# Kernel tuning notes

Measured on AMD Instinct MI355X. Metric: run time of the kernel, lower is better.

Reference implementation:

```python
import jax, jax.numpy as jnp
import numpy as np

MSA_DIM = 256
PAIR_DIM = 128
HEAD_DIM = 32


def setup_inputs() -> dict:
    key = jax.random.key(0)
    ks = jax.random.split(key, 9)
    n_seq, seq_len = 128, 256
    s = lambda d: 1.0 / np.sqrt(d)
    return {
        "msa_input": jax.random.normal(ks[0], (n_seq, seq_len, MSA_DIM), jnp.float32),
        "norm_w": jnp.ones((MSA_DIM,), jnp.float32),
        "norm_b": jnp.zeros((MSA_DIM,), jnp.float32),
        "w1": jax.random.normal(ks[1], (MSA_DIM, HEAD_DIM), jnp.float32) * s(MSA_DIM),
        "b1": jax.random.normal(ks[2], (HEAD_DIM,), jnp.float32) * 0.01,
        "w2": jax.random.normal(ks[3], (MSA_DIM, HEAD_DIM), jnp.float32) * s(MSA_DIM),
        "b2": jax.random.normal(ks[4], (HEAD_DIM,), jnp.float32) * 0.01,
        "w3": jax.random.normal(ks[5], (HEAD_DIM * HEAD_DIM, PAIR_DIM), jnp.float32) * s(HEAD_DIM * HEAD_DIM),
        "b3": jax.random.normal(ks[6], (PAIR_DIM,), jnp.float32) * 0.01,
    }


def _layernorm(x, w, b, eps=1e-5):
    mu = jnp.mean(x, axis=-1, keepdims=True)
    var = jnp.mean(jnp.square(x - mu), axis=-1, keepdims=True)
    return (x - mu) * jax.lax.rsqrt(var + eps) * w + b


def reference(msa_input, norm_w, norm_b, w1, b1, w2, b2, w3, b3):
    n_seq, seq_len, _ = msa_input.shape
    normed = _layernorm(msa_input, norm_w, norm_b)
    # proj_a uses linear2, proj_b uses linear1 (as in the torch code)
    proj_a = normed @ w2 + b2  # [n, i, c]
    proj_b = normed @ w1 + b1  # [n, j, c]
    # mean over MSA depth n expressed as a GEMM-style contraction
    outer = jnp.einsum('nia,njb->ijab', proj_a, proj_b) / n_seq  # [i, j, c, c]
    outer = outer.reshape(seq_len, seq_len, -1)
    return outer @ w3 + b3  # [i, j, pair_dim]
```

## Files before the change

kernel.cpp:

```cpp
#include <hip/hip_runtime.h>
#include <hip/hip_bf16.h>
#include <stdint.h>

#define SEQ  256
#define PD   128

typedef short bf16x8 __attribute__((ext_vector_type(8)));
typedef float f32x4  __attribute__((ext_vector_type(4)));
typedef float f32x16 __attribute__((ext_vector_type(16)));
typedef short s16x4  __attribute__((ext_vector_type(4)));

__device__ __forceinline__ short f2bf(float x) {
    union { float f; uint32_t u; } v; v.f = x;
    uint32_t r = v.u + 0x7FFFu + ((v.u >> 16) & 1u);
    return (short)(r >> 16);
}

__device__ __forceinline__ void gld16(const void* g, void* l) {
    __builtin_amdgcn_global_load_lds(
        (const __attribute__((address_space(1))) void*)g,
        (__attribute__((address_space(3))) void*)l, 16, 0, 0);
}

__global__ __launch_bounds__(256) void k_prep(const float* __restrict__ w1,
                                              const float* __restrict__ w2,
                                              const float* __restrict__ w3,
                                              short* __restrict__ w12t,
                                              short* __restrict__ w3p) {
    int id = blockIdx.x * 256 + threadIdx.x;
    if (id < 2048) {
        int col = id >> 5, cp = id & 31;
        int c = cp ^ (col & 7);
        bf16x8 o;
        #pragma unroll
        for (int e = 0; e < 8; ++e) {
            int k = c * 8 + e;
            float v = (col < 32) ? w2[k * 32 + col] : w1[k * 32 + (col - 32)];
            o[e] = f2bf(v);
        }
        *(bf16x8*)(w12t + id * 8) = o;
    } else {
        int id2 = id - 2048;
        int pg = id2 >> 12, ks = (id2 >> 6) & 63, l2 = id2 & 63;
        bf16x8 o;
        #pragma unroll
        for (int e = 0; e < 8; ++e) {
            int k = ks * 16 + (l2 >> 5) * 8 + e;
            int p = pg * 32 + (l2 & 31);
            o[e] = f2bf(w3[k * 128 + p]);
        }
        *(bf16x8*)(w3p + id2 * 8) = o;
    }
}

__global__ __launch_bounds__(256) void k_fused(const float* __restrict__ msa,
                                               const float* __restrict__ nw,
                                               const float* __restrict__ nb_,
                                               const float* __restrict__ b1,
                                               const float* __restrict__ b2,
                                               const short* __restrict__ w12t,
                                               short* __restrict__ pa,
                                               short* __restrict__ pb) {
    __shared__ short smem[32768];
    int i = blockIdx.x, nbk = blockIdx.y;
    int t = threadIdx.x, l = t & 63, w = t >> 6;

    #pragma unroll
    for (int it = 0; it < 8; ++it) {
        int ci = it * 256 + t;
        gld16(w12t + (size_t)ci * 8, smem + (it * 256 + (t & ~63)) * 8);
    }
    float4 x[16];
    const float* basep = msa + ((size_t)(nbk * 64 + w * 16) * SEQ + i) * 256 + l * 4;
    #pragma unroll
    for (int j = 0; j < 16; ++j)
        x[j] = *(const float4*)(basep + (size_t)j * SEQ * 256);
    float4 wv = *(const float4*)(nw + l * 4);
    float4 bv = *(const float4*)(nb_ + l * 4);
    #pragma unroll
    for (int j = 0; j < 16; ++j) {
        float s = x[j].x + x[j].y + x[j].z + x[j].w;
        #pragma unroll
        for (int o = 32; o > 0; o >>= 1) s += __shfl_xor(s, o, 64);
        float mu = s * (1.0f / 256.0f);
        float dx = x[j].x - mu, dy = x[j].y - mu, dz = x[j].z - mu, dw = x[j].w - mu;
        float sq = dx * dx + dy * dy + dz * dz + dw * dw;
        #pragma unroll
        for (int o = 32; o > 0; o >>= 1) sq += __shfl_xor(sq, o, 64);
        float rs = rsqrtf(sq * (1.0f / 256.0f) + 1e-5f);
        s16x4 o4;
        o4[0] = f2bf(dx * rs * wv.x + bv.x);
        o4[1] = f2bf(dy * rs * wv.y + bv.y);
        o4[2] = f2bf(dz * rs * wv.z + bv.z);
        o4[3] = f2bf(dw * rs * wv.w + bv.w);
        int row = w * 16 + j;
        *(s16x4*)((char*)smem + 32768 + row * 512 + (((l >> 1) ^ (row & 7)) * 16) + (l & 1) * 8) = o4;
    }
    __syncthreads();
    int lr = l & 15, lk = l >> 4;
    f32x4 acc[4] = {};
    #pragma unroll
    for (int ks = 0; ks < 8; ++ks) {
        int c = ks * 4 + lk;
        int xr = w * 16 + lr;
        bf16x8 xf = *(bf16x8*)((char*)smem + 32768 + xr * 512 + ((c ^ (xr & 7)) * 16));
        #pragma unroll
        for (int af = 0; af < 4; ++af) {
            int rw = af * 16 + lr;
            bf16x8 wf = *(bf16x8*)((char*)smem + rw * 512 + ((c ^ (rw & 7)) * 16));
            acc[af] = __builtin_amdgcn_mfma_f32_16x16x32_bf16(wf, xf, acc[af], 0, 0, 0);
        }
    }
    int nglob = nbk * 64 + w * 16 + lr;
    #pragma unroll
    for (int af = 0; af < 4; ++af) {
        #pragma unroll
        for (int r = 0; r < 4; ++r) {
            int cc = af * 16 + lk * 4 + r;
            float bias = (cc < 32) ? b2[cc] : b1[cc - 32];
            short v = f2bf(acc[af][r] + bias);
            if (cc < 32) pa[(size_t)(i * 32 + cc) * 128 + nglob] = v;
            else         pb[(size_t)(i * 32 + (cc - 32)) * 128 + nglob] = v;
        }
    }
}

__global__ __launch_bounds__(1024) void k_outer(const short* __restrict__ pa,
                                                const short* __restrict__ pb,
                                                const short* __restrict__ w3p,
                                                const float* __restrict__ b3,
                                                float* __restrict__ out) {
    __shared__ short smem[65536];
    int t = threadIdx.x, l = t & 63, w = t >> 6;
    int lin = blockIdx.x;
    int swz = (lin & 7) * 128 + (lin >> 3);
    int bi = swz >> 5, bj = swz & 31;

    const short* srcA = pa + (size_t)bi * 256 * 128;
    const short* srcB = pb + (size_t)bj * 256 * 128;
    #pragma unroll
    for (int it = 0; it < 8; ++it) {
        int ci = it * 1024 + t;
        int half = ci >> 12, rem = ci & 4095;
        int buf = rem >> 11, s = rem & 2047;
        int row = s >> 3, cl = s & 7;
        int gch = (cl ^ (row & 7)) + 8 * half;
        const short* g = (buf ? srcB : srcA) + row * 128 + gch * 8;
        gld16(g, smem + (it * 1024 + (t & ~63)) * 8);
    }
    __syncthreads();

    int wm = w & 3, wn = w >> 2;
    int lr = l & 15, lk = l >> 4;
    f32x4 acc1[4][4] = {};
    #pragma unroll
    for (int ks = 0; ks < 4; ++ks) {
        int c = ks * 4 + lk, half = c >> 3, cl = c & 7;
        bf16x8 af[4];
        #pragma unroll
        for (int mf = 0; mf < 4; ++mf) {
            int row = wm * 64 + mf * 16 + lr;
            af[mf] = *(bf16x8*)((char*)smem + half * 65536 + row * 128 + ((cl ^ (row & 7)) * 16));
        }
        #pragma unroll
        for (int nf = 0; nf < 4; ++nf) {
            int row = wn * 64 + nf * 16 + lr;
            bf16x8 bf = *(bf16x8*)((char*)smem + half * 65536 + 32768 + row * 128 + ((cl ^ (row & 7)) * 16));
            #pragma unroll
            for (int mf = 0; mf < 4; ++mf)
                acc1[nf][mf] = __builtin_amdgcn_mfma_f32_16x16x32_bf16(bf, af[mf], acc1[nf][mf], 0, 0, 0);
        }
    }
    __syncthreads();

    const float inv_n = 1.0f / 128.0f;
    #pragma unroll
    for (int nf = 0; nf < 4; ++nf) {
        #pragma unroll
        for (int mf = 0; mf < 4; ++mf) {
            int pair = (wm * 2 + (mf >> 1)) * 8 + (wn * 2 + (nf >> 1));
            int b = (nf & 1) * 16 + lk * 4;
            int q = lr * 4 + 2 * (nf & 1) + (lk >> 1);
            int qp = q ^ (pair & 7) ^ (((lr >> 1) & 3) << 1);
            s16x4 o;
            #pragma unroll
            for (int r = 0; r < 4; ++r) o[r] = f2bf(acc1[nf][mf][r] * inv_n);
            *(s16x4*)((char*)smem + (mf & 1) * 65536 + pair * 1024 + qp * 16 + (b & 7) * 2) = o;
        }
    }
    __syncthreads();

    f32x16 acc2[2] = {};
    int pg = w >> 1, kh = w & 1;
    if (w < 8) {
        #pragma unroll
        for (int ksi = 0; ksi < 32; ++ksi) {
            int ksg = kh * 32 + ksi;
            bf16x8 b2f = *(const bf16x8*)(w3p + ((size_t)(pg * 64 + ksg) * 64 + l) * 8);
            int q = (ksg & 31) * 2 + (l >> 5);
            int sa = (((ksg & 31) >> 2) & 3) << 1;
            #pragma unroll
            for (int mq = 0; mq < 2; ++mq) {
                int prow = mq * 32 + (l & 31);
                int qp = q ^ (prow & 7) ^ sa;
                bf16x8 a2 = *(bf16x8*)((char*)smem + kh * 65536 + prow * 1024 + qp * 16);
                acc2[mq] = __builtin_amdgcn_mfma_f32_32x32x16_bf16(a2, b2f, acc2[mq], 0, 0, 0);
            }
        }
    }
    __syncthreads();
    float* scratch = (float*)smem;
    if (w < 8 && kh == 1) {
        #pragma unroll
        for (int mq = 0; mq < 2; ++mq)
            #pragma unroll
            for (int r = 0; r < 16; ++r)
                scratch[((mq * 4 + pg) * 16 + r) * 64 + l] = acc2[mq][r];
    }
    __syncthreads();
    if (w < 8 && kh == 0) {
        float bias = b3[pg * 32 + (l & 31)];
        int p = pg * 32 + (l & 31);
        #pragma unroll
        for (int mq = 0; mq < 2; ++mq) {
            #pragma unroll
            for (int r = 0; r < 16; ++r) {
                float v = acc2[mq][r] + scratch[((mq * 4 + pg) * 16 + r) * 64 + l];
                int pair = mq * 32 + (r & 3) + 8 * (r >> 2) + 4 * (l >> 5);
                int oi = bi * 8 + (pair >> 3), oj = bj * 8 + (pair & 7);
                out[((size_t)(oi * 256 + oj)) * 128 + p] = v + bias;
            }
        }
    }
}

extern "C" void kernel_launch(void* const* d_in, const int* in_sizes, int n_in,
                              void* d_out, int out_size, void* d_ws, size_t ws_size,
                              hipStream_t stream) {
    const float* msa = (const float*)d_in[0];
    const float* nw  = (const float*)d_in[1];
    const float* nbv = (const float*)d_in[2];
    const float* w1  = (const float*)d_in[3];
    const float* b1  = (const float*)d_in[4];
    const float* w2  = (const float*)d_in[5];
    const float* b2  = (const float*)d_in[6];
    const float* w3  = (const float*)d_in[7];
    const float* b3  = (const float*)d_in[8];
    float* out = (float*)d_out;

    char* ws = (char*)d_ws;
    short* pa   = (short*)ws;
    short* pb   = (short*)(ws + (2u << 20));
    short* w3p  = (short*)(ws + (4u << 20));
    short* w12t = (short*)(ws + (4u << 20) + (256u << 10));

    k_prep <<<72, 256, 0, stream>>>(w1, w2, w3, w12t, w3p);
    k_fused<<<dim3(256, 2), 256, 0, stream>>>(msa, nw, nbv, b1, b2, w12t, pa, pb);
    k_outer<<<1024, 1024, 0, stream>>>(pa, pb, w3p, b3, out);
}
```

Before: 144.4 us.

## Split staged loads to overlap first K-half, use 32x32 MFMA, 4-way K split

The global-to-LDS staging is reordered so the first K-half arrives first. Compute on that half begins after a partial vmcnt wait while the second half is still loading. The first GEMM moves from 16x16x32 to 32x32x16 MFMA tiles and the intermediate is packed into a single 64KB region with a new swizzle. The second GEMM now runs on all 16 waves with a 4-way K split instead of 8 waves with a 2-way split, and the partial sums are reduced through LDS scratch. setprio hints are added around the MFMA blocks. The cost is a more intricate swizzle and a larger cross-wave reduction.

Result: no change. 144.8 us (+0.3%).

```diff
diff --git a/kernel.cpp b/kernel.cpp
--- a/kernel.cpp
+++ b/kernel.cpp
@@ -140,93 +140,131 @@
     const short* srcB = pb + (size_t)bj * 256 * 128;
     #pragma unroll
     for (int it = 0; it < 8; ++it) {
-        int ci = it * 1024 + t;
-        int half = ci >> 12, rem = ci & 4095;
-        int buf = rem >> 11, s = rem & 2047;
-        int row = s >> 3, cl = s & 7;
-        int gch = (cl ^ (row & 7)) + 8 * half;
-        const short* g = (buf ? srcB : srcA) + row * 128 + gch * 8;
-        gld16(g, smem + (it * 1024 + (t & ~63)) * 8);
-    }
-    __syncthreads();
+        int half = it >> 2, sub = it & 3;
+        int buf = sub >> 1;
+        int row = (sub & 1) * 128 + (t >> 3);
+        int c1  = t & 7;
+        int gch = (c1 ^ (row & 7)) + half * 8;
+        const short* g = (buf ? srcB : srcA) + (size_t)row * 128 + gch * 8;
+        int row0 = (sub & 1) * 128 + ((t & ~63) >> 3);
+        gld16(g, smem + half * 32768 + buf * 16384 + row0 * 64);
+    }
+    asm volatile("s_waitcnt vmcnt(4)" ::: "memory");
+    __builtin_amdgcn_sched_barrier(0);
+    __builtin_amdgcn_s_barrier();
+    __builtin_amdgcn_sched_barrier(0);
 
     int wm = w & 3, wn = w >> 2;
-    int lr = l & 15, lk = l >> 4;
-    f32x4 acc1[4][4] = {};
-    #pragma unroll
-    for (int ks = 0; ks < 4; ++ks) {
-        int c = ks * 4 + lk, half = c >> 3, cl = c & 7;
-        bf16x8 af[4];
-        #pragma unroll
-        for (int mf = 0; mf < 4; ++mf) {
-            int row = wm * 64 + mf * 16 + lr;
-            af[mf] = *(bf16x8*)((char*)smem + half * 65536 + row * 128 + ((cl ^ (row & 7)) * 16));
-        }
-        #pragma unroll
-        for (int nf = 0; nf < 4; ++nf) {
-            int row = wn * 64 + nf * 16 + lr;
-            bf16x8 bf = *(bf16x8*)((char*)smem + half * 65536 + 32768 + row * 128 + ((cl ^ (row & 7)) * 16));
-            #pragma unroll
-            for (int mf = 0; mf < 4; ++mf)
-                acc1[nf][mf] = __builtin_amdgcn_mfma_f32_16x16x32_bf16(bf, af[mf], acc1[nf][mf], 0, 0, 0);
-        }
+    int l31 = l & 31, lh = l >> 5;
+    f32x16 acc1[2][2] = {};
+    #pragma unroll
+    for (int ks2 = 0; ks2 < 4; ++ks2) {
+        int g = ks2 * 2 + lh, half = g >> 3, c = g & 7;
+        bf16x8 af[2], bfr[2];
+        #pragma unroll
+        for (int fm = 0; fm < 2; ++fm) {
+            int row = wm * 64 + fm * 32 + l31;
+            af[fm] = *(bf16x8*)(smem + half * 32768 + row * 64 + (c ^ (row & 7)) * 8);
+        }
+        #pragma unroll
+        for (int fn = 0; fn < 2; ++fn) {
+            int row = wn * 64 + fn * 32 + l31;
+            bfr[fn] = *(bf16x8*)(smem + half * 32768 + 16384 + row * 64 + (c ^ (row & 7)) * 8);
+        }
+        __builtin_amdgcn_s_setprio(1);
+        #pragma unroll
+        for (int fn = 0; fn < 2; ++fn)
+            #pragma unroll
+            for (int fm = 0; fm < 2; ++fm)
+                acc1[fn][fm] = __builtin_amdgcn_mfma_f32_32x32x16_bf16(bfr[fn], af[fm], acc1[fn][fm], 0, 0, 0);
+        __builtin_amdgcn_s_setprio(0);
+    }
+    __syncthreads();
+    #pragma unroll
+    for (int ks2 = 4; ks2 < 8; ++ks2) {
+        int g = ks2 * 2 + lh, half = g >> 3, c = g & 7;
+        bf16x8 af[2], bfr[2];
+        #pragma unroll
+        for (int fm = 0; fm < 2; ++fm) {
+            int row = wm * 64 + fm * 32 + l31;
+            af[fm] = *(bf16x8*)(smem + half * 32768 + row * 64 + (c ^ (row & 7)) * 8);
+        }
+        #pragma unroll
+        for (int fn = 0; fn < 2; ++fn) {
+            int row = wn * 64 + fn * 32 + l31;
+            bfr[fn] = *(bf16x8*)(smem + half * 32768 + 16384 + row * 64 + (c ^ (row & 7)) * 8);
+        }
+        __builtin_amdgcn_s_setprio(1);
+        #pragma unroll
+        for (int fn = 0; fn < 2; ++fn)
+            #pragma unroll
+            for (int fm = 0; fm < 2; ++fm)
+                acc1[fn][fm] = __builtin_amdgcn_mfma_f32_32x32x16_bf16(bfr[fn], af[fm], acc1[fn][fm], 0, 0, 0);
+        __builtin_amdgcn_s_setprio(0);
     }
     __syncthreads();
 
     const float inv_n = 1.0f / 128.0f;
     #pragma unroll
-    for (int nf = 0; nf < 4; ++nf) {
-        #pragma unroll
-        for (int mf = 0; mf < 4; ++mf) {
-            int pair = (wm * 2 + (mf >> 1)) * 8 + (wn * 2 + (nf >> 1));
-            int b = (nf & 1) * 16 + lk * 4;
-            int q = lr * 4 + 2 * (nf & 1) + (lk >> 1);
-            int qp = q ^ (pair & 7) ^ (((lr >> 1) & 3) << 1);
-            s16x4 o;
-            #pragma unroll
-            for (int r = 0; r < 4; ++r) o[r] = f2bf(acc1[nf][mf][r] * inv_n);
-            *(s16x4*)((char*)smem + (mf & 1) * 65536 + pair * 1024 + qp * 16 + (b & 7) * 2) = o;
-        }
-    }
-    __syncthreads();
-
+    for (int fn = 0; fn < 2; ++fn) {
+        #pragma unroll
+        for (int fm = 0; fm < 2; ++fm) {
+            int pair = (wm * 2 + fm) * 8 + wn * 2 + fn;
+            #pragma unroll
+            for (int g = 0; g < 4; ++g) {
+                int q  = l31 * 4 + g;
+                int qp = q ^ (pair & 7) ^ ((q >> 3) & 7);
+                s16x4 o;
+                #pragma unroll
+                for (int j = 0; j < 4; ++j) o[j] = f2bf(acc1[fn][fm][g * 4 + j] * inv_n);
+                *(s16x4*)(smem + pair * 1024 + qp * 8 + lh * 4) = o;
+            }
+        }
+    }
+    __syncthreads();
+
+    int pg = w & 3, kh = w >> 2;
     f32x16 acc2[2] = {};
-    int pg = w >> 1, kh = w & 1;
-    if (w < 8) {
-        #pragma unroll
-        for (int ksi = 0; ksi < 32; ++ksi) {
-            int ksg = kh * 32 + ksi;
-            bf16x8 b2f = *(const bf16x8*)(w3p + ((size_t)(pg * 64 + ksg) * 64 + l) * 8);
-            int q = (ksg & 31) * 2 + (l >> 5);
-            int sa = (((ksg & 31) >> 2) & 3) << 1;
-            #pragma unroll
-            for (int mq = 0; mq < 2; ++mq) {
-                int prow = mq * 32 + (l & 31);
-                int qp = q ^ (prow & 7) ^ sa;
-                bf16x8 a2 = *(bf16x8*)((char*)smem + kh * 65536 + prow * 1024 + qp * 16);
-                acc2[mq] = __builtin_amdgcn_mfma_f32_32x32x16_bf16(a2, b2f, acc2[mq], 0, 0, 0);
-            }
-        }
-    }
-    __syncthreads();
+    __builtin_amdgcn_s_setprio(1);
+    #pragma unroll
+    for (int ksi = 0; ksi < 16; ++ksi) {
+        int ksg = kh * 16 + ksi;
+        bf16x8 b2f = *(const bf16x8*)(w3p + ((size_t)(pg * 64 + ksg) * 64 + l) * 8);
+        int qr  = ksg * 2 + lh;
+        int sig = (ksg >> 2) & 7;
+        #pragma unroll
+        for (int mq = 0; mq < 2; ++mq) {
+            int prow = mq * 32 + l31;
+            int qp = qr ^ (prow & 7) ^ sig;
+            bf16x8 a2 = *(bf16x8*)(smem + prow * 1024 + qp * 8);
+            acc2[mq] = __builtin_amdgcn_mfma_f32_32x32x16_bf16(a2, b2f, acc2[mq], 0, 0, 0);
+        }
+    }
+    __builtin_amdgcn_s_setprio(0);
+    __syncthreads();
+
     float* scratch = (float*)smem;
-    if (w < 8 && kh == 1) {
+    if (kh != 0) {
+        int base = ((kh - 1) * 4 + pg) * 2;
         #pragma unroll
         for (int mq = 0; mq < 2; ++mq)
             #pragma unroll
             for (int r = 0; r < 16; ++r)
-                scratch[((mq * 4 + pg) * 16 + r) * 64 + l] = acc2[mq][r];
-    }
-    __syncthreads();
-    if (w < 8 && kh == 0) {
-        float bias = b3[pg * 32 + (l & 31)];
-        int p = pg * 32 + (l & 31);
+                scratch[((base + mq) * 16 + r) * 64 + l] = acc2[mq][r];
+    }
+    __syncthreads();
+    if (kh == 0) {
+        int p = pg * 32 + l31;
+        float bias = b3[p];
         #pragma unroll
         for (int mq = 0; mq < 2; ++mq) {
             #pragma unroll
             for (int r = 0; r < 16; ++r) {
-                float v = acc2[mq][r] + scratch[((mq * 4 + pg) * 16 + r) * 64 + l];
-                int pair = mq * 32 + (r & 3) + 8 * (r >> 2) + 4 * (l >> 5);
+                float v = acc2[mq][r];
+                #pragma unroll
+                for (int kk = 0; kk < 3; ++kk)
+                    v += scratch[(((kk * 4 + pg) * 2 + mq) * 16 + r) * 64 + l];
+                int pair = mq * 32 + (r & 3) + 8 * (r >> 2) + 4 * lh;
                 int oi = bi * 8 + (pair >> 3), oj = bj * 8 + (pair & 7);
                 out[((size_t)(oi * 256 + oj)) * 128 + p] = v + bias;
             }
```
